# Performance work log

Measured on AMD Instinct MI355X. Metric: run time of the kernel, lower is better.

## Reference

```python
import jax, jax.numpy as jnp
import numpy as np

N, E = 20000, 320000
EPS = 1e-5
NEG_SLOPE = 0.2


def gat_conv(x, src, dst, W, att_src, att_dst, bias, num_nodes):
    # W: [Fin, H*C], att_*: [H, C], bias: [H*C]
    H, C = att_src.shape
    h = (x @ W).reshape(num_nodes, H, C)            # [N,H,C]
    a_s = jnp.einsum('nhc,hc->nh', h, att_src)      # [N,H]
    a_d = jnp.einsum('nhc,hc->nh', h, att_dst)      # [N,H]
    e = jax.nn.leaky_relu(a_s[src] + a_d[dst], NEG_SLOPE)  # [E,H]
    m = jax.ops.segment_max(e, dst, num_segments=num_nodes)       # per-dst max (self-loops guarantee non-empty)
    ex = jnp.exp(e - m[dst])
    s = jax.ops.segment_sum(ex, dst, num_segments=num_nodes)
    alpha = ex / s[dst]                              # [E,H] segment softmax
    out = jax.ops.segment_sum(h[src] * alpha[:, :, None], dst, num_segments=num_nodes)  # [N,H,C]
    return out.reshape(num_nodes, H * C) + bias


def batch_norm(x, gamma, beta):
    mu = x.mean(axis=0)
    var = x.var(axis=0)  # biased, as torch BN uses for normalization
    return (x - mu) * jax.lax.rsqrt(var + EPS) * gamma + beta


def setup_inputs() -> dict:
    key = jax.random.key(0)
    ks = jax.random.split(key, 32)
    x = jax.random.normal(ks[0], (N, 512), dtype=jnp.float32)
    edge_index = jax.random.randint(ks[1], (2, E), 0, N, dtype=jnp.int32)
    d = {"x": x, "edge_index": edge_index}
    # layer configs: (Fin, C_out, H)
    cfgs = [(512, 64, 8), (512, 64, 4), (256, 64, 2), (128, 16, 1)]
    i = 2
    for li, (fin, c, h) in enumerate(cfgs, start=1):
        sc = 1.0 / np.sqrt(fin)
        d[f"W{li}"] = jax.random.normal(ks[i], (fin, h * c), dtype=jnp.float32) * sc; i += 1
        d[f"as{li}"] = jax.random.normal(ks[i], (h, c), dtype=jnp.float32) * 0.1; i += 1
        d[f"ad{li}"] = jax.random.normal(ks[i], (h, c), dtype=jnp.float32) * 0.1; i += 1
        d[f"b{li}"] = jnp.zeros((h * c,), dtype=jnp.float32)
        if li < 4:
            d[f"g{li}"] = jnp.ones((h * c,), dtype=jnp.float32)
            d[f"be{li}"] = jnp.zeros((h * c,), dtype=jnp.float32)
    return d


def reference(x, edge_index, W1, as1, ad1, b1, g1, be1, W2, as2, ad2, b2, g2, be2, W3, as3, ad3, b3, g3, be3, W4, as4, ad4, b4):
    num_nodes = x.shape[0]
    loop = jnp.arange(num_nodes, dtype=edge_index.dtype)
    src = jnp.concatenate([edge_index[0], loop])  # add_self_loops=True
    dst = jnp.concatenate([edge_index[1], loop])
    h = gat_conv(x, src, dst, W1, as1, ad1, b1, num_nodes)
    h = jax.nn.elu(batch_norm(h, g1, be1))
    h = gat_conv(h, src, dst, W2, as2, ad2, b2, num_nodes)
    h = jax.nn.elu(batch_norm(h, g2, be2))
    h = gat_conv(h, src, dst, W3, as3, ad3, b3, num_nodes)
    h = jax.nn.elu(batch_norm(h, g3, be3))
    h = gat_conv(h, src, dst, W4, as4, ad4, b4, num_nodes)
    return jax.nn.log_softmax(h, axis=1)
```

## Files before the change

kernel.cpp:

```cpp
#include <hip/hip_runtime.h>
#include <hip/hip_bf16.h>
#include <cstdint>
#include <cstddef>

#define NN 20000
#define EE 320000
#define ET (EE + NN)
#define MPAD 20096
#define SCHUNK 20

typedef __attribute__((ext_vector_type(8))) short  short8;
typedef __attribute__((ext_vector_type(4))) float  floatx4;

__device__ inline unsigned short f2bf(float f) {
    unsigned u = __float_as_uint(f);
    u += 0x7FFFu + ((u >> 16) & 1u);
    return (unsigned short)(u >> 16);
}
__device__ inline float bf2f(unsigned short b) {
    return __uint_as_float(((unsigned)b) << 16);
}
__device__ inline float bflo(unsigned u) { return __uint_as_float(u << 16); }
__device__ inline float bfhi(unsigned u) { return __uint_as_float(u & 0xFFFF0000u); }

__global__ void zero_i32(int* __restrict__ p, int n) {
    int i = blockIdx.x * blockDim.x + threadIdx.x;
    if (i < n) p[i] = 0;
}

#define W1SZ (512 * 512)
#define W2SZ (512 * 256)
#define W3SZ (256 * 128)
#define NW_BLOCKS ((W1SZ + W2SZ + W3SZ) / 256)
__global__ void cvt_w_all(const float* __restrict__ W1, unsigned short* __restrict__ Wt1,
                          const float* __restrict__ W2, unsigned short* __restrict__ Wt2,
                          const float* __restrict__ W3, unsigned short* __restrict__ Wt3) {
    int i = blockIdx.x * blockDim.x + threadIdx.x;
    const float* W; unsigned short* Wt; int K, N, idx;
    if (i < W1SZ)                    { W = W1; Wt = Wt1; K = 512; N = 512; idx = i; }
    else if (i < W1SZ + W2SZ)        { W = W2; Wt = Wt2; K = 512; N = 256; idx = i - W1SZ; }
    else if (i < W1SZ + W2SZ + W3SZ) { W = W3; Wt = Wt3; K = 256; N = 128; idx = i - W1SZ - W2SZ; }
    else return;
    int k = idx / N, n = idx - k * N;
    Wt[(size_t)n * K + k] = f2bf(W[idx]);
}

__global__ void count_edges(const int* __restrict__ dst, int* __restrict__ cnt) {
    int e = blockIdx.x * blockDim.x + threadIdx.x;
    if (e >= ET) return;
    int d = (e < EE) ? dst[e] : (e - EE);
    atomicAdd(&cnt[d], 1);
}

__global__ __launch_bounds__(1024) void scan_fast(const int* __restrict__ cnt,
                                                  int* __restrict__ rowp,
                                                  int* __restrict__ wptr, int n) {
    __shared__ int sums[1024];
    const int t = threadIdx.x;
    const int base = t * SCHUNK;
    int local[SCHUNK];
    int acc = 0;
#pragma unroll
    for (int i = 0; i < SCHUNK; ++i) {
        int idx = base + i;
        int v = (idx < n) ? cnt[idx] : 0;
        local[i] = acc;
        acc += v;
    }
    sums[t] = acc;
    __syncthreads();
    for (int o = 1; o < 1024; o <<= 1) {
        int u = (t >= o) ? sums[t - o] : 0;
        __syncthreads();
        sums[t] += u;
        __syncthreads();
    }
    int excl = sums[t] - acc;
#pragma unroll
    for (int i = 0; i < SCHUNK; ++i) {
        int idx = base + i;
        if (idx < n) { int rp = excl + local[i]; rowp[idx] = rp; wptr[idx] = rp; }
    }
    if (t == 1023) rowp[n] = sums[1023];
}

__global__ void fill_edges(const int* __restrict__ src, const int* __restrict__ dst,
                           int* __restrict__ wptr, int* __restrict__ colx) {
    int e = blockIdx.x * blockDim.x + threadIdx.x;
    if (e >= ET) return;
    int s, d;
    if (e < EE) { s = src[e]; d = dst[e]; } else { s = e - EE; d = e - EE; }
    int pos = atomicAdd(&wptr[d], 1);
    colx[pos] = s;
}

template <int MODE>
__global__ __launch_bounds__(256) void gemm_bf16_fused(
        const float* __restrict__ A, const unsigned short* __restrict__ Bt,
        unsigned short* __restrict__ hN, float* __restrict__ aS, float* __restrict__ aD,
        const float* __restrict__ atts, const float* __restrict__ attd,
        const float* __restrict__ ssg,
        int M, int N, int K, int Mreal, int gxsh, int gy) {
    __shared__ unsigned short As[128][42];
    __shared__ unsigned short Bs[128][42];
    __shared__ float ssS[512];
    __shared__ float ssH[512];

    const int lid = blockIdx.x;
    const int c8 = lid & 7, kk = lid >> 3;
    const int bx = kk & ((1 << gxsh) - 1);
    const int by = c8 + 8 * (kk >> gxsh);
    if (by >= gy) return;

    const int t = threadIdx.x;
    const int lane = t & 63, wave = t >> 6;
    const int wm = wave >> 1, wn = wave & 1;
    const int quad = lane >> 4, mrow = lane & 15;
    const int row0 = by * 128, col0 = bx * 128;
    const int srow = t >> 2, schunk = (t & 3) * 8;

    if constexpr (MODE == 2) {
        for (int i = t; i < K; i += 256) { ssS[i] = ssg[i]; ssH[i] = ssg[K + i]; }
        __syncthreads();
    }

    floatx4 acc[4][4];
#pragma unroll
    for (int i = 0; i < 4; ++i)
#pragma unroll
        for (int j = 0; j < 4; ++j)
#pragma unroll
            for (int r = 0; r < 4; ++r) acc[i][j][r] = 0.f;

    for (int k0 = 0; k0 < K; k0 += 32) {
        float sc[8], sh[8];
        if constexpr (MODE == 2) {
#pragma unroll
            for (int i = 0; i < 8; ++i) { sc[i] = ssS[k0 + schunk + i]; sh[i] = ssH[k0 + schunk + i]; }
        }
        auto stage_row = [&](int arow) -> uint4 {
            uint4 r = make_uint4(0u, 0u, 0u, 0u);
            if (arow < Mreal) {
                float4 f0 = *(const float4*)(A + (size_t)arow * K + k0 + schunk);
                float4 f1 = *(const float4*)(A + (size_t)arow * K + k0 + schunk + 4);
                float v[8] = { f0.x, f0.y, f0.z, f0.w, f1.x, f1.y, f1.z, f1.w };
                unsigned short h[8];
#pragma unroll
                for (int i = 0; i < 8; ++i) {
                    float u = v[i];
                    if constexpr (MODE == 2) {
                        u = u * sc[i] + sh[i];
                        u = (u > 0.f) ? u : (__expf(u) - 1.f);
                    }
                    h[i] = f2bf(u);
                }
                r = make_uint4((unsigned)h[0] | ((unsigned)h[1] << 16),
                               (unsigned)h[2] | ((unsigned)h[3] << 16),
                               (unsigned)h[4] | ((unsigned)h[5] << 16),
                               (unsigned)h[6] | ((unsigned)h[7] << 16));
            }
            return r;
        };
        uint4 ra0 = stage_row(row0 + srow);
        uint4 ra1 = stage_row(row0 + srow + 64);
        uint4 rb0 = *(const uint4*)(Bt + (size_t)(col0 + srow)      * K + k0 + schunk);
        uint4 rb1 = *(const uint4*)(Bt + (size_t)(col0 + srow + 64) * K + k0 + schunk);
        __syncthreads();
        *(uint4*)&As[srow][schunk]      = ra0;
        *(uint4*)&As[srow + 64][schunk] = ra1;
        *(uint4*)&Bs[srow][schunk]      = rb0;
        *(uint4*)&Bs[srow + 64][schunk] = rb1;
        __syncthreads();

        short8 af[4], bfr[4];
#pragma unroll
        for (int i = 0; i < 4; ++i)
            af[i] = *(const short8*)&As[wm * 64 + i * 16 + mrow][quad * 8];
#pragma unroll
        for (int j = 0; j < 4; ++j)
            bfr[j] = *(const short8*)&Bs[wn * 64 + j * 16 + mrow][quad * 8];
#pragma unroll
        for (int i = 0; i < 4; ++i)
#pragma unroll
            for (int j = 0; j < 4; ++j)
                acc[i][j] = __builtin_amdgcn_mfma_f32_16x16x32_bf16(af[i], bfr[j], acc[i][j], 0, 0, 0);
    }

    const int head = (col0 + wn * 64) >> 6;
    float attS[4], attD[4];
#pragma unroll
    for (int j = 0; j < 4; ++j) {
        attS[j] = atts[head * 64 + j * 16 + mrow];
        attD[j] = attd[head * 64 + j * 16 + mrow];
    }

#pragma unroll
    for (int i = 0; i < 4; ++i) {
#pragma unroll
        for (int r = 0; r < 4; ++r) {
            int row = row0 + wm * 64 + i * 16 + quad * 4 + r;
            float ps = acc[i][0][r] * attS[0] + acc[i][1][r] * attS[1]
                     + acc[i][2][r] * attS[2] + acc[i][3][r] * attS[3];
            float pd = acc[i][0][r] * attD[0] + acc[i][1][r] * attD[1]
                     + acc[i][2][r] * attD[2] + acc[i][3][r] * attD[3];
#pragma unroll
            for (int o = 1; o < 16; o <<= 1) {
                ps += __shfl_xor(ps, o);
                pd += __shfl_xor(pd, o);
            }
            if (row < M) {
                if (mrow == 0) {
                    aS[(size_t)head * M + row] = ps;
                    aD[(size_t)head * M + row] = pd;
                }
#pragma unroll
                for (int j = 0; j < 4; ++j)
                    hN[(size_t)row * N + col0 + wn * 64 + j * 16 + mrow] = f2bf(acc[i][j][r]);
            }
        }
    }
}

template <int HH>
__global__ __launch_bounds__(256) void gat_agg_head32(
        const unsigned short* __restrict__ hN,
        const float* __restrict__ aS, const float* __restrict__ aD,
        const int* __restrict__ rowp, const int* __restrict__ colx,
        const float* __restrict__ bias, float* __restrict__ out,
        float* __restrict__ part, int Nn) {
    constexpr int F = HH * 64;
    constexpr unsigned F2 = F * 2;
    constexpr int G = 8 / HH;
    __shared__ uint2 pair[4][4][33];
    __shared__ float red[4][16][9];
    const int L = blockIdx.x;
    const int x8 = L & 7;
    const int hd = x8 / G;
    const int nodeblk = (L >> 3) * G + (x8 & (G - 1));
    const int wave = threadIdx.x >> 6, lane = threadIdx.x & 63;
    const int grp = lane >> 4;
    const int q   = lane & 15;
    const int eo  = q >> 3;
    const int lo  = (q & 7) * 16;
    const int n = nodeblk * 16 + wave * 4 + grp;
    const bool valid = (n < Nn);

    const char* hb = (const char*)hN + hd * 128;

    float a0 = 0.f, a1 = 0.f, a2 = 0.f, a3 = 0.f;
    float a4 = 0.f, a5 = 0.f, a6 = 0.f, a7 = 0.f;
    float4 o4 = make_float4(0.f, 0.f, 0.f, 0.f);

    if (valid) {
        const float* aSh = aS + (size_t)hd * Nn;
        const float adv = aD[(size_t)hd * Nn + n];
        const int b0 = rowp[n], b1 = rowp[n + 1];

        float m, s;

        auto gather = [&](int cnt) {
            for (int j = 0; j < cnt; j += 8) {
                uint2 x0 = pair[wave][grp][j + eo + 0];
                uint2 x1 = pair[wave][grp][j + eo + 2];
                uint2 x2 = pair[wave][grp][j + eo + 4];
                uint2 x3 = pair[wave][grp][j + eo + 6];
                uint4 v0 = *(const uint4*)(hb + x0.x + lo);
                uint4 v1 = *(const uint4*)(hb + x1.x + lo);
                uint4 v2 = *(const uint4*)(hb + x2.x + lo);
                uint4 v3 = *(const uint4*)(hb + x3.x + lo);
                float p0 = __uint_as_float(x0.y), p1 = __uint_as_float(x1.y);
                float p2 = __uint_as_float(x2.y), p3 = __uint_as_float(x3.y);
                a0 += p0 * bflo(v0.x) + p1 * bflo(v1.x) + p2 * bflo(v2.x) + p3 * bflo(v3.x);
                a1 += p0 * bfhi(v0.x) + p1 * bfhi(v1.x) + p2 * bfhi(v2.x) + p3 * bfhi(v3.x);
                a2 += p0 * bflo(v0.y) + p1 * bflo(v1.y) + p2 * bflo(v2.y) + p3 * bflo(v3.y);
                a3 += p0 * bfhi(v0.y) + p1 * bfhi(v1.y) + p2 * bfhi(v2.y) + p3 * bfhi(v3.y);
                a4 += p0 * bflo(v0.z) + p1 * bflo(v1.z) + p2 * bflo(v2.z) + p3 * bflo(v3.z);
                a5 += p0 * bfhi(v0.z) + p1 * bfhi(v1.z) + p2 * bfhi(v2.z) + p3 * bfhi(v3.z);
                a6 += p0 * bflo(v0.w) + p1 * bflo(v1.w) + p2 * bflo(v2.w) + p3 * bflo(v3.w);
                a7 += p0 * bfhi(v0.w) + p1 * bfhi(v1.w) + p2 * bfhi(v2.w) + p3 * bfhi(v3.w);
            }
        };

        {
            const int cnt = min(32, b1 - b0);
            int sn0 = 0, sn1 = 0;
            if (q < cnt)      sn0 = colx[b0 + q];
            if (q + 16 < cnt) sn1 = colx[b0 + q + 16];
            float t0 = aSh[sn0] + adv;
            float t1 = aSh[sn1] + adv;
            float e0 = (q < cnt)      ? ((t0 > 0.f) ? t0 : 0.2f * t0) : -1e30f;
            float e1 = (q + 16 < cnt) ? ((t1 > 0.f) ? t1 : 0.2f * t1) : -1e30f;
            float mc = fmaxf(e0, e1);
#pragma unroll
            for (int o = 8; o > 0; o >>= 1) mc = fmaxf(mc, __shfl_xor(mc, o));
            m = mc;
            float p0 = __expf(e0 - m);
            float p1 = __expf(e1 - m);
            float ps = p0 + p1;
#pragma unroll
            for (int o = 8; o > 0; o >>= 1) ps += __shfl_xor(ps, o);
            s = ps;
            pair[wave][grp][q]      = make_uint2((unsigned)sn0 * F2, __float_as_uint(p0));
            pair[wave][grp][q + 16] = make_uint2((unsigned)sn1 * F2, __float_as_uint(p1));
            __threadfence_block();
            gather(cnt);
        }

        for (int c0 = b0 + 32; c0 < b1; c0 += 32) {
            __threadfence_block();
            const int cnt = min(32, b1 - c0);
            int sn0 = 0, sn1 = 0;
            if (q < cnt)      sn0 = colx[c0 + q];
            if (q + 16 < cnt) sn1 = colx[c0 + q + 16];
            float t0 = aSh[sn0] + adv;
            float t1 = aSh[sn1] + adv;
            float e0 = (q < cnt)      ? ((t0 > 0.f) ? t0 : 0.2f * t0) : -1e30f;
            float e1 = (q + 16 < cnt) ? ((t1 > 0.f) ? t1 : 0.2f * t1) : -1e30f;
            float mc = fmaxf(e0, e1);
#pragma unroll
            for (int o = 8; o > 0; o >>= 1) mc = fmaxf(mc, __shfl_xor(mc, o));
            float nm = fmaxf(m, mc);
            float sc = __expf(m - nm);
            float p0 = __expf(e0 - nm);
            float p1 = __expf(e1 - nm);
            float ps = p0 + p1;
#pragma unroll
            for (int o = 8; o > 0; o >>= 1) ps += __shfl_xor(ps, o);
            s = s * sc + ps;
            a0 *= sc; a1 *= sc; a2 *= sc; a3 *= sc;
            a4 *= sc; a5 *= sc; a6 *= sc; a7 *= sc;
            m = nm;
            pair[wave][grp][q]      = make_uint2((unsigned)sn0 * F2, __float_as_uint(p0));
            pair[wave][grp][q + 16] = make_uint2((unsigned)sn1 * F2, __float_as_uint(p1));
            __threadfence_block();
            gather(cnt);
        }

        a0 += __shfl_xor(a0, 8); a1 += __shfl_xor(a1, 8);
        a2 += __shfl_xor(a2, 8); a3 += __shfl_xor(a3, 8);
        a4 += __shfl_xor(a4, 8); a5 += __shfl_xor(a5, 8);
        a6 += __shfl_xor(a6, 8); a7 += __shfl_xor(a7, 8);

        const float inv = 1.f / s;
        float r0 = eo ? a4 : a0;
        float r1 = eo ? a5 : a1;
        float r2 = eo ? a6 : a2;
        float r3 = eo ? a7 : a3;
        const int cb = hd * 64 + (q & 7) * 8 + eo * 4;
        o4.x = r0 * inv + bias[cb + 0];
        o4.y = r1 * inv + bias[cb + 1];
        o4.z = r2 * inv + bias[cb + 2];
        o4.w = r3 * inv + bias[cb + 3];
        *(float4*)(out + (size_t)n * F + cb) = o4;
    }

    float s0 = o4.x, s1 = o4.y, s2 = o4.z, s3 = o4.w;
    float q0 = s0 * s0, q1 = s1 * s1, q2 = s2 * s2, q3 = s3 * s3;
#pragma unroll
    for (int o = 16; o < 64; o <<= 1) {
        s0 += __shfl_xor(s0, o); s1 += __shfl_xor(s1, o);
        s2 += __shfl_xor(s2, o); s3 += __shfl_xor(s3, o);
        q0 += __shfl_xor(q0, o); q1 += __shfl_xor(q1, o);
        q2 += __shfl_xor(q2, o); q3 += __shfl_xor(q3, o);
    }
    if (grp == 0) {
        red[wave][q][0] = s0; red[wave][q][1] = s1;
        red[wave][q][2] = s2; red[wave][q][3] = s3;
        red[wave][q][4] = q0; red[wave][q][5] = q1;
        red[wave][q][6] = q2; red[wave][q][7] = q3;
    }
    __syncthreads();
    if (wave == 0 && lane < 16) {
        float a[8];
#pragma unroll
        for (int k = 0; k < 8; ++k)
            a[k] = red[0][q][k] + red[1][q][k] + red[2][q][k] + red[3][q][k];
        const int cq = (q & 7) * 2 + eo;
        float* pb = part + (size_t)L * 128;
#pragma unroll
        for (int k = 0; k < 4; ++k) {
            pb[cq * 4 + k]      = a[k];
            pb[64 + cq * 4 + k] = a[4 + k];
        }
    }
}

__global__ __launch_bounds__(256) void gemm_l4_fused(const float* __restrict__ A,
                                                     const float* __restrict__ B,
                                                     unsigned short* __restrict__ C,
                                                     float* __restrict__ aS, float* __restrict__ aD,
                                                     const float* __restrict__ atts,
                                                     const float* __restrict__ attd,
                                                     const float* __restrict__ ssg,
                                                     int M, int N, int K, int Mreal) {
    __shared__ float As[16][65];
    __shared__ float Bs[16][64];
    const int tid = threadIdx.x;
    const int tx = tid & 15, ty = tid >> 4;
    const int row0 = blockIdx.y * 64, col0 = blockIdx.x * 64;
    const int rA = tid >> 2, kq = (tid & 3) << 2;
    const int rB = tid >> 4, cq = (tid & 15) << 2;
    float acc[4][4] = {};

    for (int k0 = 0; k0 < K; k0 += 16) {
        const int arow = row0 + rA;
        float a0v = 0.f, a1v = 0.f, a2v = 0.f, a3v = 0.f;
        if (arow < Mreal) {
            float4 fa = *(const float4*)(A + (size_t)arow * K + k0 + kq);
            const int c = k0 + kq;
            a0v = fa.x * ssg[c + 0] + ssg[K + c + 0];
            a1v = fa.y * ssg[c + 1] + ssg[K + c + 1];
            a2v = fa.z * ssg[c + 2] + ssg[K + c + 2];
            a3v = fa.w * ssg[c + 3] + ssg[K + c + 3];
            a0v = (a0v > 0.f) ? a0v : (__expf(a0v) - 1.f);
            a1v = (a1v > 0.f) ? a1v : (__expf(a1v) - 1.f);
            a2v = (a2v > 0.f) ? a2v : (__expf(a2v) - 1.f);
            a3v = (a3v > 0.f) ? a3v : (__expf(a3v) - 1.f);
        }
        float4 fb = make_float4(0.f, 0.f, 0.f, 0.f);
        int bcol = col0 + cq;
        if (bcol < N) fb = *(const float4*)(B + (size_t)(k0 + rB) * N + bcol);
        As[kq + 0][rA] = a0v; As[kq + 1][rA] = a1v;
        As[kq + 2][rA] = a2v; As[kq + 3][rA] = a3v;
        *(float4*)&Bs[rB][cq] = fb;
        __syncthreads();
#pragma unroll
        for (int k = 0; k < 16; ++k) {
            float a0 = As[k][ty * 4 + 0];
            float a1 = As[k][ty * 4 + 1];
            float a2 = As[k][ty * 4 + 2];
            float a3 = As[k][ty * 4 + 3];
            float4 b = *(float4*)&Bs[k][tx * 4];
            acc[0][0] += a0 * b.x; acc[0][1] += a0 * b.y; acc[0][2] += a0 * b.z; acc[0][3] += a0 * b.w;
            acc[1][0] += a1 * b.x; acc[1][1] += a1 * b.y; acc[1][2] += a1 * b.z; acc[1][3] += a1 * b.w;
            acc[2][0] += a2 * b.x; acc[2][1] += a2 * b.y; acc[2][2] += a2 * b.z; acc[2][3] += a2 * b.w;
            acc[3][0] += a3 * b.x; acc[3][1] += a3 * b.y; acc[3][2] += a3 * b.z; acc[3][3] += a3 * b.w;
        }
        __syncthreads();
    }
    float as_part[4], ad_part[4];
#pragma unroll
    for (int i = 0; i < 4; ++i) { as_part[i] = 0.f; ad_part[i] = 0.f; }
    if (tx < 4) {
#pragma unroll
        for (int i = 0; i < 4; ++i) {
#pragma unroll
            for (int jj = 0; jj < 4; ++jj) {
                int c = tx * 4 + jj;
                as_part[i] += acc[i][jj] * atts[c];
                ad_part[i] += acc[i][jj] * attd[c];
            }
        }
    }
#pragma unroll
    for (int i = 0; i < 4; ++i) {
        float ps = as_part[i], pd = ad_part[i];
        ps += __shfl_xor(ps, 1); ps += __shfl_xor(ps, 2);
        pd += __shfl_xor(pd, 1); pd += __shfl_xor(pd, 2);
        int r = row0 + ty * 4 + i;
        if (r < M) {
            if (tx == 0) { aS[r] = ps; aD[r] = pd; }
#pragma unroll
            for (int jj = 0; jj < 4; ++jj) {
                int c = col0 + tx * 4 + jj;
                if (c < N) C[(size_t)r * N + c] = f2bf(acc[i][jj]);
            }
        }
    }
}

template <int C>
__global__ void gat_agg_l4_ls(const unsigned short* __restrict__ ht,
                              const float* __restrict__ as, const float* __restrict__ aD,
                              const int* __restrict__ rowp, const int* __restrict__ colx,
                              const float* __restrict__ bias, float* __restrict__ out, int Nn) {
    int n = blockIdx.x * 4 + (threadIdx.x >> 6);
    int lane = threadIdx.x & 63;
    if (n >= Nn) return;
    float adv = aD[n];
    int b0 = rowp[n], b1 = rowp[n + 1];

    float m = -1e30f, s = 0.f, acc = 0.f;
    for (int c0 = b0; c0 < b1; c0 += 64) {
        int cnt = b1 - c0; if (cnt > 64) cnt = 64;
        int sn = 0; float e = -1e30f;
        if (lane < cnt) {
            sn = colx[c0 + lane];
            float tt = as[sn] + adv;
            e = (tt > 0.f) ? tt : 0.2f * tt;
        }
        float mc = e;
#pragma unroll
        for (int o = 32; o > 0; o >>= 1) mc = fmaxf(mc, __shfl_xor(mc, o));
        float nm = fmaxf(m, mc);
        float sc = __expf(m - nm);
        acc *= sc; s *= sc;
        float p = (lane < cnt) ? __expf(e - nm) : 0.f;
        float ps = p;
#pragma unroll
        for (int o = 32; o > 0; o >>= 1) ps += __shfl_xor(ps, o);
        s += ps; m = nm;

        int j = 0;
        for (; j + 4 <= cnt; j += 4) {
            int s0 = __shfl(sn, j),     s1 = __shfl(sn, j + 1);
            int s2 = __shfl(sn, j + 2), s3 = __shfl(sn, j + 3);
            float p0 = __shfl(p, j),     p1 = __shfl(p, j + 1);
            float p2 = __shfl(p, j + 2), p3 = __shfl(p, j + 3);
            float h0 = 0.f, h1 = 0.f, h2 = 0.f, h3 = 0.f;
            if (lane < C) {
                h0 = bf2f(ht[(size_t)s0 * C + lane]);
                h1 = bf2f(ht[(size_t)s1 * C + lane]);
                h2 = bf2f(ht[(size_t)s2 * C + lane]);
                h3 = bf2f(ht[(size_t)s3 * C + lane]);
            }
            acc += p0 * h0 + p1 * h1 + p2 * h2 + p3 * h3;
        }
        for (; j < cnt; ++j) {
            int sj = __shfl(sn, j);
            float pj = __shfl(p, j);
            float hv = (lane < C) ? bf2f(ht[(size_t)sj * C + lane]) : 0.f;
            acc += pj * hv;
        }
    }
    float v = (lane < C) ? (acc / s + bias[lane]) : -1e30f;
    float mx = v;
#pragma unroll
    for (int o = 8; o > 0; o >>= 1) mx = fmaxf(mx, __shfl_xor(mx, o));
    float ex = (lane < C) ? __expf(v - mx) : 0.f;
#pragma unroll
    for (int o = 8; o > 0; o >>= 1) ex += __shfl_xor(ex, o);
    float l = __logf(ex) + mx;
    if (lane < C) out[(size_t)n * C + lane] = v - l;
}

template <int F>
__global__ __launch_bounds__(1024) void bn_reduce_par(const float* __restrict__ part,
                                                      const float* __restrict__ gamma,
                                                      const float* __restrict__ beta,
                                                      float* __restrict__ ss,
                                                      float invN, int NB8) {
    constexpr int G = 512 / F;
    __shared__ float sd[32][33];
    const int t = threadIdx.x;
    const int pr = t >> 5;
    const int tg = t & 31;
    const int c0 = blockIdx.x * 16;
    const int c  = c0 + (tg & 15);
    const int hd = c >> 6;
    const int off = (c & 63) + ((tg < 16) ? 0 : 64);
    float a0 = 0.f, a1 = 0.f, a2 = 0.f, a3 = 0.f;
    for (int g = 0; g < G; ++g) {
        const float* pb = part + (size_t)(hd * G + g) * 128 + off;
        int j = pr;
        for (; j + 96 < NB8; j += 128) {
            a0 += pb[(size_t)(j +  0) * 1024];
            a1 += pb[(size_t)(j + 32) * 1024];
            a2 += pb[(size_t)(j + 64) * 1024];
            a3 += pb[(size_t)(j + 96) * 1024];
        }
        for (; j < NB8; j += 32)
            a0 += pb[(size_t)j * 1024];
    }
    sd[pr][tg] = (a0 + a1) + (a2 + a3);
    __syncthreads();
    if (pr == 0) {
        float tot = sd[0][tg];
#pragma unroll
        for (int r = 1; r < 32; ++r) tot += sd[r][tg];
        sd[0][tg] = tot;
    }
    __syncthreads();
    if (t < 16) {
        int cc = c0 + t;
        float s = sd[0][t];
        float q = sd[0][16 + t];
        float mu = s * invN;
        float var = q * invN - mu * mu;
        float sc = gamma[cc] * rsqrtf(var + 1e-5f);
        ss[cc] = sc;
        ss[F + cc] = beta[cc] - mu * sc;
    }
}

extern "C" void kernel_launch(void* const* d_in, const int* in_sizes, int n_in,
                              void* d_out, int out_size, void* d_ws, size_t ws_size,
                              hipStream_t stream) {
    const float* x   = (const float*)d_in[0];
    const int*   ei  = (const int*)d_in[1];
    const float* W1  = (const float*)d_in[2];
    const float* as1 = (const float*)d_in[3];
    const float* ad1 = (const float*)d_in[4];
    const float* b1  = (const float*)d_in[5];
    const float* ga1 = (const float*)d_in[6];
    const float* be1 = (const float*)d_in[7];
    const float* W2  = (const float*)d_in[8];
    const float* as2 = (const float*)d_in[9];
    const float* ad2 = (const float*)d_in[10];
    const float* b2  = (const float*)d_in[11];
    const float* ga2 = (const float*)d_in[12];
    const float* be2 = (const float*)d_in[13];
    const float* W3  = (const float*)d_in[14];
    const float* as3 = (const float*)d_in[15];
    const float* ad3 = (const float*)d_in[16];
    const float* b3  = (const float*)d_in[17];
    const float* ga3 = (const float*)d_in[18];
    const float* be3 = (const float*)d_in[19];
    const float* W4  = (const float*)d_in[20];
    const float* as4 = (const float*)d_in[21];
    const float* ad4 = (const float*)d_in[22];
    const float* b4  = (const float*)d_in[23];
    float* outp = (float*)d_out;

    uint8_t* base = (uint8_t*)d_ws;
    size_t off = 0;
    auto alloc = [&](size_t nbytes) -> void* {
        off = (off + 255) & ~(size_t)255;
        void* p = base + off;
        off += nbytes;
        return p;
    };
    float* bufO = (float*)alloc((size_t)NN * 512 * 4);
    unsigned short* hN   = (unsigned short*)alloc((size_t)NN * 512 * 2);
    unsigned short* Wt1  = (unsigned short*)alloc((size_t)512 * 512 * 2);
    unsigned short* Wt2  = (unsigned short*)alloc((size_t)256 * 512 * 2);
    unsigned short* Wt3  = (unsigned short*)alloc((size_t)128 * 256 * 2);
    float* aSn  = (float*)alloc((size_t)NN * 8 * 4);
    float* aDn  = (float*)alloc((size_t)NN * 8 * 4);
    int*   cnt  = (int*)alloc((size_t)NN * 4);
    int*   rowp = (int*)alloc((size_t)(NN + 1) * 4);
    int*   wptr = (int*)alloc((size_t)NN * 4);
    int*   colx = (int*)alloc((size_t)ET * 4);
    float* bnp  = (float*)alloc((size_t)10048 * 128 * 4);
    float* bns  = (float*)alloc((size_t)1024 * 4);

    const int* srcRow = ei;
    const int* dstRow = ei + EE;

    zero_i32<<<(NN + 255) / 256, 256, 0, stream>>>(cnt, NN);
    count_edges<<<(ET + 255) / 256, 256, 0, stream>>>(dstRow, cnt);
    scan_fast<<<1, 1024, 0, stream>>>(cnt, rowp, wptr, NN);
    fill_edges<<<(ET + 255) / 256, 256, 0, stream>>>(srcRow, dstRow, wptr, colx);

    cvt_w_all<<<NW_BLOCKS, 256, 0, stream>>>(W1, Wt1, W2, Wt2, W3, Wt3);

    const int NBLK = (NN + 15) / 16;
    const int GY8 = 160;

    {
        gemm_bf16_fused<1><<<4 * GY8, 256, 0, stream>>>(x, Wt1, hN, aSn, aDn, as1, ad1,
                                                        nullptr, NN, 512, 512, NN, 2, 157);
        gat_agg_head32<8><<<NBLK * 8, 256, 0, stream>>>(hN, aSn, aDn, rowp, colx, b1, bufO, bnp, NN);
        bn_reduce_par<512><<<512 / 16, 1024, 0, stream>>>(bnp, ga1, be1, bns, 1.0f / NN, NBLK);
    }
    {
        gemm_bf16_fused<2><<<2 * GY8, 256, 0, stream>>>(bufO, Wt2, hN, aSn, aDn, as2, ad2,
                                                        bns, NN, 256, 512, NN, 1, 157);
        const int nb8 = (NBLK + 1) / 2;
        gat_agg_head32<4><<<nb8 * 8, 256, 0, stream>>>(hN, aSn, aDn, rowp, colx, b2, bufO, bnp, NN);
        bn_reduce_par<256><<<256 / 16, 1024, 0, stream>>>(bnp, ga2, be2, bns, 1.0f / NN, nb8);
    }
    {
        gemm_bf16_fused<2><<<1 * GY8, 256, 0, stream>>>(bufO, Wt3, hN, aSn, aDn, as3, ad3,
                                                        bns, NN, 128, 256, NN, 0, 157);
        const int nb8 = (NBLK + 3) / 4;
        gat_agg_head32<2><<<nb8 * 8, 256, 0, stream>>>(hN, aSn, aDn, rowp, colx, b3, bufO, bnp, NN);
        bn_reduce_par<128><<<128 / 16, 1024, 0, stream>>>(bnp, ga3, be3, bns, 1.0f / NN, nb8);
    }
    {
        dim3 g(1, (NN + 63) / 64);
        gemm_l4_fused<<<g, 256, 0, stream>>>(bufO, W4, hN, aSn, aDn, as4, ad4,
                                             bns, NN, 16, 128, NN);
        gat_agg_l4_ls<16><<<(NN + 3) / 4, 256, 0, stream>>>(hN, aSn, aDn, rowp, colx, b4, outp, NN);
    }
}
```

Measured before the change: 402.2 us.

## Pre-pack GEMM operands into MFMA-fragment-ordered bf16 tiles in separate kernels

Moves the fp32-to-bf16 conversion and the BN+ELU prologue out of the GEMM into separate prep kernels. These write A and B as contiguous 128x32 tiles already ordered to match the MFMA fragment layout. The GEMM inner loop then does fully coalesced 16-byte loads and conflict-free LDS reads with no per-element math. The cost is an extra pass over the activations per layer, with extra launches and extra global write and read traffic, in exchange for a simpler and faster GEMM main loop.

```diff
diff --git a/kernel.cpp b/kernel.cpp
--- a/kernel.cpp
+++ b/kernel.cpp
@@ -23,26 +23,98 @@
 __device__ inline float bflo(unsigned u) { return __uint_as_float(u << 16); }
 __device__ inline float bfhi(unsigned u) { return __uint_as_float(u & 0xFFFF0000u); }
 
+__device__ inline void chunk_decode(int ch, int& rl, int& kl) {
+    const int wm = ch >> 8, i = (ch >> 6) & 3, quad = (ch >> 4) & 3, mrow = ch & 15;
+    rl = wm * 64 + i * 16 + mrow;
+    kl = quad * 8;
+}
+__device__ inline uint4 pack8(const float* v) {
+    unsigned short h[8];
+#pragma unroll
+    for (int e = 0; e < 8; ++e) h[e] = f2bf(v[e]);
+    return make_uint4((unsigned)h[0] | ((unsigned)h[1] << 16),
+                      (unsigned)h[2] | ((unsigned)h[3] << 16),
+                      (unsigned)h[4] | ((unsigned)h[5] << 16),
+                      (unsigned)h[6] | ((unsigned)h[7] << 16));
+}
+
 __global__ void zero_i32(int* __restrict__ p, int n) {
     int i = blockIdx.x * blockDim.x + threadIdx.x;
     if (i < n) p[i] = 0;
 }
 
-#define W1SZ (512 * 512)
-#define W2SZ (512 * 256)
-#define W3SZ (256 * 128)
-#define NW_BLOCKS ((W1SZ + W2SZ + W3SZ) / 256)
-__global__ void cvt_w_all(const float* __restrict__ W1, unsigned short* __restrict__ Wt1,
-                          const float* __restrict__ W2, unsigned short* __restrict__ Wt2,
-                          const float* __restrict__ W3, unsigned short* __restrict__ Wt3) {
-    int i = blockIdx.x * blockDim.x + threadIdx.x;
-    const float* W; unsigned short* Wt; int K, N, idx;
-    if (i < W1SZ)                    { W = W1; Wt = Wt1; K = 512; N = 512; idx = i; }
-    else if (i < W1SZ + W2SZ)        { W = W2; Wt = Wt2; K = 512; N = 256; idx = i - W1SZ; }
-    else if (i < W1SZ + W2SZ + W3SZ) { W = W3; Wt = Wt3; K = 256; N = 128; idx = i - W1SZ - W2SZ; }
-    else return;
-    int k = idx / N, n = idx - k * N;
-    Wt[(size_t)n * K + k] = f2bf(W[idx]);
+#define NA_CHUNKS (157 * 16 * 512)
+#define NA_BLOCKS (NA_CHUNKS / 256)
+#define W1C (4 * 16 * 512)
+#define W2C (2 * 16 * 512)
+#define W3C (1 * 8 * 512)
+#define NW_BLOCKS ((W1C + W2C + W3C) / 256)
+__global__ void prep_all(const float* __restrict__ x, unsigned short* __restrict__ Ap,
+                         const float* __restrict__ W1, unsigned short* __restrict__ Wt1,
+                         const float* __restrict__ W2, unsigned short* __restrict__ Wt2,
+                         const float* __restrict__ W3, unsigned short* __restrict__ Wt3) {
+    const int b = blockIdx.x;
+    if (b < NA_BLOCKS) {
+        const int c = b * 256 + threadIdx.x;
+        const int rt = c >> 13;
+        const int rem = c & 8191;
+        const int ks = rem >> 9, ch = rem & 511;
+        int rl, kl; chunk_decode(ch, rl, kl);
+        const int row = rt * 128 + rl;
+        const int k = ks * 32 + kl;
+        uint4 o = make_uint4(0u, 0u, 0u, 0u);
+        if (row < NN) {
+            float4 f0 = *(const float4*)(x + (size_t)row * 512 + k);
+            float4 f1 = *(const float4*)(x + (size_t)row * 512 + k + 4);
+            float v[8] = { f0.x, f0.y, f0.z, f0.w, f1.x, f1.y, f1.z, f1.w };
+            o = pack8(v);
+        }
+        *(uint4*)(Ap + (size_t)c * 8) = o;
+    } else {
+        int i2 = (b - NA_BLOCKS) * 256 + threadIdx.x;
+        const float* W; unsigned short* Wt; int Nw, KSw, c;
+        if (i2 < W1C)              { W = W1; Wt = Wt1; Nw = 512; KSw = 16; c = i2; }
+        else if (i2 < W1C + W2C)   { W = W2; Wt = Wt2; Nw = 256; KSw = 16; c = i2 - W1C; }
+        else                       { W = W3; Wt = Wt3; Nw = 128; KSw = 8;  c = i2 - W1C - W2C; }
+        const int cpt = KSw * 512;
+        const int nt = c / cpt;
+        const int rem = c - nt * cpt;
+        const int ks = rem >> 9, ch = rem & 511;
+        int rl, kl; chunk_decode(ch, rl, kl);
+        const int n = nt * 128 + rl;
+        const int k = ks * 32 + kl;
+        float v[8];
+#pragma unroll
+        for (int e = 0; e < 8; ++e) v[e] = W[(size_t)(k + e) * Nw + n];
+        *(uint4*)(Wt + (size_t)c * 8) = pack8(v);
+    }
+}
+
+template <int F>
+__global__ void bn_apply_perm(const float* __restrict__ xin, const float* __restrict__ ss,
+                              unsigned short* __restrict__ Ap, int Nn) {
+    constexpr int CPT = (F / 32) * 512;
+    constexpr int SH = (F == 512) ? 13 : 12;
+    const int c = blockIdx.x * 256 + threadIdx.x;
+    const int rt = c >> SH;
+    const int rem = c & (CPT - 1);
+    const int ks = rem >> 9, ch = rem & 511;
+    int rl, kl; chunk_decode(ch, rl, kl);
+    const int row = rt * 128 + rl;
+    const int k = ks * 32 + kl;
+    uint4 o = make_uint4(0u, 0u, 0u, 0u);
+    if (row < Nn) {
+        float4 f0 = *(const float4*)(xin + (size_t)row * F + k);
+        float4 f1 = *(const float4*)(xin + (size_t)row * F + k + 4);
+        float v[8] = { f0.x, f0.y, f0.z, f0.w, f1.x, f1.y, f1.z, f1.w };
+#pragma unroll
+        for (int e = 0; e < 8; ++e) {
+            float u = v[e] * ss[k + e] + ss[F + k + e];
+            v[e] = (u > 0.f) ? u : (__expf(u) - 1.f);
+        }
+        o = pack8(v);
+    }
+    *(uint4*)(Ap + (size_t)c * 8) = o;
 }
 
 __global__ void count_edges(const int* __restrict__ dst, int* __restrict__ cnt) {
@@ -94,22 +166,18 @@
     colx[pos] = s;
 }
 
-template <int MODE>
 __global__ __launch_bounds__(256) void gemm_bf16_fused(
-        const float* __restrict__ A, const unsigned short* __restrict__ Bt,
+        const unsigned short* __restrict__ Ap, const unsigned short* __restrict__ Btp,
         unsigned short* __restrict__ hN, float* __restrict__ aS, float* __restrict__ aD,
         const float* __restrict__ atts, const float* __restrict__ attd,
-        const float* __restrict__ ssg,
-        int M, int N, int K, int Mreal, int gxsh, int gy) {
-    __shared__ unsigned short As[128][42];
-    __shared__ unsigned short Bs[128][42];
-    __shared__ float ssS[512];
-    __shared__ float ssH[512];
+        int M, int N, int K, int gxsh, int gy) {
+    __shared__ unsigned short As[4096];
+    __shared__ unsigned short Bs[4096];
 
     const int lid = blockIdx.x;
-    const int c8 = lid & 7, kk = lid >> 3;
-    const int bx = kk & ((1 << gxsh) - 1);
-    const int by = c8 + 8 * (kk >> gxsh);
+    const int c8 = lid & 7, kkk = lid >> 3;
+    const int bx = kkk & ((1 << gxsh) - 1);
+    const int by = c8 + 8 * (kkk >> gxsh);
     if (by >= gy) return;
 
     const int t = threadIdx.x;
@@ -117,68 +185,37 @@
     const int wm = wave >> 1, wn = wave & 1;
     const int quad = lane >> 4, mrow = lane & 15;
     const int row0 = by * 128, col0 = bx * 128;
-    const int srow = t >> 2, schunk = (t & 3) * 8;
-
-    if constexpr (MODE == 2) {
-        for (int i = t; i < K; i += 256) { ssS[i] = ssg[i]; ssH[i] = ssg[K + i]; }
+    const int KSn = K >> 5;
+
+    floatx4 acc[4][4];
+#pragma unroll
+    for (int i = 0; i < 4; ++i)
+#pragma unroll
+        for (int j = 0; j < 4; ++j)
+#pragma unroll
+            for (int r = 0; r < 4; ++r) acc[i][j][r] = 0.f;
+
+    for (int kk = 0; kk < KSn; ++kk) {
+        const size_t ab = ((size_t)(by * KSn + kk) * 512) * 8;
+        const size_t bb = ((size_t)(bx * KSn + kk) * 512) * 8;
+        uint4 ra0 = *(const uint4*)(Ap  + ab + (size_t)t * 8);
+        uint4 ra1 = *(const uint4*)(Ap  + ab + (size_t)(t + 256) * 8);
+        uint4 rb0 = *(const uint4*)(Btp + bb + (size_t)t * 8);
+        uint4 rb1 = *(const uint4*)(Btp + bb + (size_t)(t + 256) * 8);
         __syncthreads();
-    }
-
-    floatx4 acc[4][4];
-#pragma unroll
-    for (int i = 0; i < 4; ++i)
+        *(uint4*)&As[t * 8]         = ra0;
+        *(uint4*)&As[(t + 256) * 8] = ra1;
+        *(uint4*)&Bs[t * 8]         = rb0;
+        *(uint4*)&Bs[(t + 256) * 8] = rb1;
+        __syncthreads();
+
+        short8 af[4], bfr[4];
+#pragma unroll
+        for (int i = 0; i < 4; ++i)
+            af[i] = *(const short8*)&As[(wm * 256 + i * 64 + lane) * 8];
 #pragma unroll
         for (int j = 0; j < 4; ++j)
-#pragma unroll
-            for (int r = 0; r < 4; ++r) acc[i][j][r] = 0.f;
-
-    for (int k0 = 0; k0 < K; k0 += 32) {
-        float sc[8], sh[8];
-        if constexpr (MODE == 2) {
-#pragma unroll
-            for (int i = 0; i < 8; ++i) { sc[i] = ssS[k0 + schunk + i]; sh[i] = ssH[k0 + schunk + i]; }
-        }
-        auto stage_row = [&](int arow) -> uint4 {
-            uint4 r = make_uint4(0u, 0u, 0u, 0u);
-            if (arow < Mreal) {
-                float4 f0 = *(const float4*)(A + (size_t)arow * K + k0 + schunk);
-                float4 f1 = *(const float4*)(A + (size_t)arow * K + k0 + schunk + 4);
-                float v[8] = { f0.x, f0.y, f0.z, f0.w, f1.x, f1.y, f1.z, f1.w };
-                unsigned short h[8];
-#pragma unroll
-                for (int i = 0; i < 8; ++i) {
-                    float u = v[i];
-                    if constexpr (MODE == 2) {
-                        u = u * sc[i] + sh[i];
-                        u = (u > 0.f) ? u : (__expf(u) - 1.f);
-                    }
-                    h[i] = f2bf(u);
-                }
-                r = make_uint4((unsigned)h[0] | ((unsigned)h[1] << 16),
-                               (unsigned)h[2] | ((unsigned)h[3] << 16),
-                               (unsigned)h[4] | ((unsigned)h[5] << 16),
-                               (unsigned)h[6] | ((unsigned)h[7] << 16));
-            }
-            return r;
-        };
-        uint4 ra0 = stage_row(row0 + srow);
-        uint4 ra1 = stage_row(row0 + srow + 64);
-        uint4 rb0 = *(const uint4*)(Bt + (size_t)(col0 + srow)      * K + k0 + schunk);
-        uint4 rb1 = *(const uint4*)(Bt + (size_t)(col0 + srow + 64) * K + k0 + schunk);
-        __syncthreads();
-        *(uint4*)&As[srow][schunk]      = ra0;
-        *(uint4*)&As[srow + 64][schunk] = ra1;
-        *(uint4*)&Bs[srow][schunk]      = rb0;
-        *(uint4*)&Bs[srow + 64][schunk] = rb1;
-        __syncthreads();
-
-        short8 af[4], bfr[4];
-#pragma unroll
-        for (int i = 0; i < 4; ++i)
-            af[i] = *(const short8*)&As[wm * 64 + i * 16 + mrow][quad * 8];
-#pragma unroll
-        for (int j = 0; j < 4; ++j)
-            bfr[j] = *(const short8*)&Bs[wn * 64 + j * 16 + mrow][quad * 8];
+            bfr[j] = *(const short8*)&Bs[(wn * 256 + j * 64 + lane) * 8];
 #pragma unroll
         for (int i = 0; i < 4; ++i)
 #pragma unroll
@@ -621,10 +658,11 @@
         return p;
     };
     float* bufO = (float*)alloc((size_t)NN * 512 * 4);
+    unsigned short* Ap   = (unsigned short*)alloc((size_t)NA_CHUNKS * 8 * 2);
     unsigned short* hN   = (unsigned short*)alloc((size_t)NN * 512 * 2);
-    unsigned short* Wt1  = (unsigned short*)alloc((size_t)512 * 512 * 2);
-    unsigned short* Wt2  = (unsigned short*)alloc((size_t)256 * 512 * 2);
-    unsigned short* Wt3  = (unsigned short*)alloc((size_t)128 * 256 * 2);
+    unsigned short* Wt1  = (unsigned short*)alloc((size_t)W1C * 8 * 2);
+    unsigned short* Wt2  = (unsigned short*)alloc((size_t)W2C * 8 * 2);
+    unsigned short* Wt3  = (unsigned short*)alloc((size_t)W3C * 8 * 2);
     float* aSn  = (float*)alloc((size_t)NN * 8 * 4);
     float* aDn  = (float*)alloc((size_t)NN * 8 * 4);
     int*   cnt  = (int*)alloc((size_t)NN * 4);
@@ -642,27 +680,29 @@
     scan_fast<<<1, 1024, 0, stream>>>(cnt, rowp, wptr, NN);
     fill_edges<<<(ET + 255) / 256, 256, 0, stream>>>(srcRow, dstRow, wptr, colx);
 
-    cvt_w_all<<<NW_BLOCKS, 256, 0, stream>>>(W1, Wt1, W2, Wt2, W3, Wt3);
+    prep_all<<<NA_BLOCKS + NW_BLOCKS, 256, 0, stream>>>(x, Ap, W1, Wt1, W2, Wt2, W3, Wt3);
 
     const int NBLK = (NN + 15) / 16;
     const int GY8 = 160;
 
     {
-        gemm_bf16_fused<1><<<4 * GY8, 256, 0, stream>>>(x, Wt1, hN, aSn, aDn, as1, ad1,
-                                                        nullptr, NN, 512, 512, NN, 2, 157);
+        gemm_bf16_fused<<<4 * GY8, 256, 0, stream>>>(Ap, Wt1, hN, aSn, aDn, as1, ad1,
+                                                     NN, 512, 512, 2, 157);
         gat_agg_head32<8><<<NBLK * 8, 256, 0, stream>>>(hN, aSn, aDn, rowp, colx, b1, bufO, bnp, NN);
         bn_reduce_par<512><<<512 / 16, 1024, 0, stream>>>(bnp, ga1, be1, bns, 1.0f / NN, NBLK);
     }
     {
-        gemm_bf16_fused<2><<<2 * GY8, 256, 0, stream>>>(bufO, Wt2, hN, aSn, aDn, as2, ad2,
-                                                        bns, NN, 256, 512, NN, 1, 157);
+        bn_apply_perm<512><<<(157 * 16 * 512) / 256, 256, 0, stream>>>(bufO, bns, Ap, NN);
+        gemm_bf16_fused<<<2 * GY8, 256, 0, stream>>>(Ap, Wt2, hN, aSn, aDn, as2, ad2,
+                                                     NN, 256, 512, 1, 157);
         const int nb8 = (NBLK + 1) / 2;
         gat_agg_head32<4><<<nb8 * 8, 256, 0, stream>>>(hN, aSn, aDn, rowp, colx, b2, bufO, bnp, NN);
         bn_reduce_par<256><<<256 / 16, 1024, 0, stream>>>(bnp, ga2, be2, bns, 1.0f / NN, nb8);
     }
     {
-        gemm_bf16_fused<2><<<1 * GY8, 256, 0, stream>>>(bufO, Wt3, hN, aSn, aDn, as3, ad3,
-                                                        bns, NN, 128, 256, NN, 0, 157);
+        bn_apply_perm<256><<<(157 * 8 * 512) / 256, 256, 0, stream>>>(bufO, bns, Ap, NN);
+        gemm_bf16_fused<<<1 * GY8, 256, 0, stream>>>(Ap, Wt3, hN, aSn, aDn, as3, ad3,
+                                                     NN, 128, 256, 0, 157);
         const int nb8 = (NBLK + 3) / 4;
         gat_agg_head32<2><<<nb8 * 8, 256, 0, stream>>>(hN, aSn, aDn, rowp, colx, b3, bufO, bnp, NN);
         bn_reduce_par<128><<<128 / 16, 1024, 0, stream>>>(bnp, ga3, be3, bns, 1.0f / NN, nb8);
```

Measured after the change: 390.6 us (median of 2 runs). 1.03x faster.
